# Performance work log

Hardware: AMD Instinct MI355X
Metric: run time of the kernel (lower is better)

## Reference

```python
import jax, jax.numpy as jnp
import numpy as np

BITS, NF, NX = 8, 4096, 1024
G = NX // 8  # groups of 8 weights packed per uint8


def setup_inputs() -> dict:
    key = jax.random.key(0)
    k1, k2, k3, k4 = jax.random.split(key, 4)
    x = jax.random.normal(k1, (2, 2048, NX), dtype=jnp.float32)
    # packed sign bytes per (bit-plane, out-feature, group-of-8 inputs)
    binary = jax.random.randint(k2, (BITS, NF, G), 0, 256, dtype=jnp.int32)
    # per-bit-plane, per-output-row scale (always positive in the sup/l2 schemes)
    scale = jax.random.uniform(k3, (BITS, NF, 1), dtype=jnp.float32)
    bias = jax.random.normal(k4, (NF,), dtype=jnp.float32)
    return {"x": x, "binary": binary, "scale": scale, "bias": bias}


def _decode_signs(binary):
    # binary_exp in the torch code is [2^7..2^0], so element j of each group of 8
    # is stored in bit (7 - j). map4 maps a set bit -> +1, clear bit -> -1.
    shifts = jnp.arange(7, -1, -1, dtype=binary.dtype)
    bits = (binary[..., None] >> shifts) & 1  # (BITS, NF, G, 8)
    sign = jnp.where(bits == 1, 1.0, -1.0).astype(jnp.float32)
    return sign.reshape(binary.shape[0], binary.shape[1], -1)  # (BITS, NF, NX)


def reference(x, binary, scale, bias):
    # Math of the original forward:
    #   table[t, g, hi, lo] = x[t, 8g:8g+4] . map4[:, hi] + x[t, 8g+4:8g+8] . map4[:, lo]
    #   out[t, f] = sum_i scale[i, f] * sum_g table[t, g, binary[i,f,g]>>4, binary[i,f,g]&15]
    # which is exactly sum_i scale[i,f] * (x[t] . sign_i[f]).  We fold the
    # bit-plane sum into an effective weight and run one dense GEMM.
    size_out = x.shape[:-1] + (scale.shape[1],)
    xf = x.reshape(-1, x.shape[-1])            # (T, NX)
    sign = _decode_signs(binary)               # (BITS, NF, NX), values in {-1,+1}
    W = jnp.einsum('kfn,kfo->fn', sign, scale)  # effective weight (NF, NX)
    out = xf @ W.T + bias                      # (T, NF)
    return out.reshape(size_out)
```

## Files before the change

### kernel.cpp

```cpp
#include <hip/hip_runtime.h>
#include <hip/hip_bf16.h>
#include <stdint.h>


#define BITS 8
#define NF   4096
#define NXX  1024
#define GRP  (NXX / 8)

#define BM 256
#define BN 256
#define BK 64
#define NTHR 512

typedef __attribute__((ext_vector_type(4))) float f32x4;
typedef __attribute__((ext_vector_type(8))) short bf16x8;

__global__ __launch_bounds__(256) void k_prep(const float* __restrict__ x,
                                              const int* __restrict__ binary,
                                              const float* __restrict__ scale,
                                              __hip_bfloat16* __restrict__ xb,
                                              __hip_bfloat16* __restrict__ Wb) {
    const int b = blockIdx.x;
    const int tid = threadIdx.x;
    if (b < 2048) {
        int i = b * 256 + tid;
        const float4* xp = (const float4*)x;
        float4 a = xp[2 * i], c = xp[2 * i + 1];
        union { __hip_bfloat16 h[8]; int4 v; } u;
        u.h[0] = __float2bfloat16(a.x);
        u.h[1] = __float2bfloat16(a.y);
        u.h[2] = __float2bfloat16(a.z);
        u.h[3] = __float2bfloat16(a.w);
        u.h[4] = __float2bfloat16(c.x);
        u.h[5] = __float2bfloat16(c.y);
        u.h[6] = __float2bfloat16(c.z);
        u.h[7] = __float2bfloat16(c.w);
        ((int4*)xb)[i] = u.v;
    } else {
        int idx = (b - 2048) * 256 + tid;
        int f = idx >> 7;
        int g = idx & (GRP - 1);
        float sc[BITS];
        int   bv[BITS];
#pragma unroll
        for (int k = 0; k < BITS; ++k) {
            sc[k] = scale[k * NF + f];
            bv[k] = binary[(size_t)(k * NF + f) * GRP + g];
        }
        union { __hip_bfloat16 h[8]; int4 v; } u;
#pragma unroll
        for (int j = 0; j < 8; ++j) {
            float s = 0.f;
#pragma unroll
            for (int k = 0; k < BITS; ++k)
                s += ((bv[k] >> (7 - j)) & 1) ? sc[k] : -sc[k];
            u.h[j] = __float2bfloat16(s);
        }
        ((int4*)Wb)[idx] = u.v;
    }
}

__global__ __launch_bounds__(NTHR, 2) void k_gemm(const __hip_bfloat16* __restrict__ A,
                                                  const __hip_bfloat16* __restrict__ B,
                                                  const float* __restrict__ bias,
                                                  float* __restrict__ C,
                                                  int M, int N, int K) {
    __shared__ __align__(16) char lds[131072];

    const int tid  = threadIdx.x;
    const int lane = tid & 63;
    const int wid  = tid >> 6;
    const int wm = wid >> 2;
    const int wn = wid & 3;
    const int lr = lane & 15;
    const int lk = lane >> 4;

    const int nwg = gridDim.x;
    const int cpx = nwg >> 3;
    const int bid = blockIdx.x;
    const int swz = (bid & 7) * cpx + (bid >> 3);
    const int m0 = (swz >> 4) * BM;
    const int n0 = (swz & 15) * BN;

    const int NT = K / BK;

    auto stageA = [&](int buf, int kt) {
        const __hip_bfloat16* src = A + (size_t)m0 * K + kt;
        char* dst = lds + buf * 65536;
#pragma unroll
        for (int j = 0; j < 4; ++j) {
            int c = j * 512 + tid;
            int r = c >> 3;
            int q = (c & 7) ^ (r & 7);
            __builtin_amdgcn_global_load_lds(
                (const __attribute__((address_space(1))) void*)(src + (size_t)r * K + q * 8),
                (__attribute__((address_space(3))) void*)(dst + j * 8192 + tid * 16), 16, 0, 0);
        }
    };
    auto stageB = [&](int buf, int kt) {
        const __hip_bfloat16* src = B + (size_t)n0 * K + kt;
        char* dst = lds + buf * 65536 + 32768;
#pragma unroll
        for (int j = 0; j < 4; ++j) {
            int c = j * 512 + tid;
            int r = c >> 3;
            int q = (c & 7) ^ (r & 7);
            __builtin_amdgcn_global_load_lds(
                (const __attribute__((address_space(1))) void*)(src + (size_t)r * K + q * 8),
                (__attribute__((address_space(3))) void*)(dst + j * 8192 + tid * 16), 16, 0, 0);
        }
    };
    auto ldA = [&](int buf, int msub, int i, int kk) -> bf16x8 {
        int R = wm * 128 + msub * 64 + i * 16 + lr;
        int CB = (kk * 64 + lk * 16) ^ ((R & 7) << 4);
        return *(const bf16x8*)(lds + buf * 65536 + R * 128 + CB);
    };
    auto ldB = [&](int buf, int nsub, int j, int kk) -> bf16x8 {
        int R = wn * 64 + nsub * 32 + j * 16 + lr;
        int CB = (kk * 64 + lk * 16) ^ ((R & 7) << 4);
        return *(const bf16x8*)(lds + buf * 65536 + 32768 + R * 128 + CB);
    };

    f32x4 acc[8][4] = {};
    bf16x8 aF[4][2], bF0[2][2], bF1[2][2];

    stageA(0, 0);
    stageB(0, 0);

    for (int t = 0; t < NT; ++t) {
        const int cb = t & 1;
        const bool st = (t + 1 < NT);
        asm volatile("s_waitcnt vmcnt(0)" ::: "memory");
        __builtin_amdgcn_sched_barrier(0);
        __builtin_amdgcn_s_barrier();

#pragma unroll
        for (int i = 0; i < 4; ++i)
#pragma unroll
            for (int kk = 0; kk < 2; ++kk) aF[i][kk] = ldA(cb, 0, i, kk);
#pragma unroll
        for (int j = 0; j < 2; ++j)
#pragma unroll
            for (int kk = 0; kk < 2; ++kk) bF0[j][kk] = ldB(cb, 0, j, kk);
        if (st) stageA(cb ^ 1, (t + 1) * BK);
        __builtin_amdgcn_s_barrier();
        asm volatile("s_waitcnt lgkmcnt(0)" ::: "memory");
        __builtin_amdgcn_sched_barrier(0);
        __builtin_amdgcn_s_setprio(1);
#pragma unroll
        for (int i = 0; i < 4; ++i)
#pragma unroll
            for (int j = 0; j < 2; ++j)
#pragma unroll
                for (int kk = 0; kk < 2; ++kk)
                    acc[i][j] = __builtin_amdgcn_mfma_f32_16x16x32_bf16(aF[i][kk], bF0[j][kk], acc[i][j], 0, 0, 0);
        __builtin_amdgcn_s_setprio(0);
        __builtin_amdgcn_sched_barrier(0);
        __builtin_amdgcn_s_barrier();

#pragma unroll
        for (int j = 0; j < 2; ++j)
#pragma unroll
            for (int kk = 0; kk < 2; ++kk) bF1[j][kk] = ldB(cb, 1, j, kk);
        if (st) stageB(cb ^ 1, (t + 1) * BK);
        __builtin_amdgcn_s_barrier();
        asm volatile("s_waitcnt lgkmcnt(0)" ::: "memory");
        __builtin_amdgcn_sched_barrier(0);
        __builtin_amdgcn_s_setprio(1);
#pragma unroll
        for (int i = 0; i < 4; ++i)
#pragma unroll
            for (int j = 0; j < 2; ++j)
#pragma unroll
                for (int kk = 0; kk < 2; ++kk)
                    acc[i][2 + j] = __builtin_amdgcn_mfma_f32_16x16x32_bf16(aF[i][kk], bF1[j][kk], acc[i][2 + j], 0, 0, 0);
        __builtin_amdgcn_s_setprio(0);
        __builtin_amdgcn_sched_barrier(0);
        __builtin_amdgcn_s_barrier();

#pragma unroll
        for (int i = 0; i < 4; ++i)
#pragma unroll
            for (int kk = 0; kk < 2; ++kk) aF[i][kk] = ldA(cb, 1, i, kk);
        __builtin_amdgcn_s_barrier();
        asm volatile("s_waitcnt lgkmcnt(0)" ::: "memory");
        __builtin_amdgcn_sched_barrier(0);
        __builtin_amdgcn_s_setprio(1);
#pragma unroll
        for (int i = 0; i < 4; ++i)
#pragma unroll
            for (int j = 0; j < 2; ++j)
#pragma unroll
                for (int kk = 0; kk < 2; ++kk)
                    acc[4 + i][j] = __builtin_amdgcn_mfma_f32_16x16x32_bf16(aF[i][kk], bF0[j][kk], acc[4 + i][j], 0, 0, 0);
        __builtin_amdgcn_s_setprio(0);
        __builtin_amdgcn_sched_barrier(0);
        __builtin_amdgcn_s_barrier();

        __builtin_amdgcn_s_setprio(1);
#pragma unroll
        for (int i = 0; i < 4; ++i)
#pragma unroll
            for (int j = 0; j < 2; ++j)
#pragma unroll
                for (int kk = 0; kk < 2; ++kk)
                    acc[4 + i][2 + j] = __builtin_amdgcn_mfma_f32_16x16x32_bf16(aF[i][kk], bF1[j][kk], acc[4 + i][2 + j], 0, 0, 0);
        __builtin_amdgcn_s_setprio(0);
        __builtin_amdgcn_sched_barrier(0);
        __builtin_amdgcn_s_barrier();
    }

#pragma unroll
    for (int j = 0; j < 4; ++j) {
        int col = n0 + wn * 64 + j * 16 + lr;
        float bv = bias[col];
#pragma unroll
        for (int i = 0; i < 8; ++i) {
            int row = m0 + wm * 128 + i * 16 + lk * 4;
#pragma unroll
            for (int r = 0; r < 4; ++r)
                C[(size_t)(row + r) * N + col] = acc[i][j][r] + bv;
        }
    }
}

extern "C" void kernel_launch(void* const* d_in, const int* in_sizes, int n_in,
                              void* d_out, int out_size, void* d_ws, size_t ws_size,
                              hipStream_t stream) {
    const float* x      = (const float*)d_in[0];
    const int*   binary = (const int*)d_in[1];
    const float* scale  = (const float*)d_in[2];
    const float* bias   = (const float*)d_in[3];
    float* out = (float*)d_out;

    const int M = in_sizes[0] / NXX;

    __hip_bfloat16* xb = (__hip_bfloat16*)d_ws;
    __hip_bfloat16* Wb = xb + (size_t)M * NXX;

    k_prep<<<2048 + (NF * GRP) / 256, 256, 0, stream>>>(x, binary, scale, xb, Wb);
    k_gemm<<<(M / BM) * (NF / BN), NTHR, 0, stream>>>(xb, Wb, bias, out, M, NF, NXX);
}
```

Measured before the change: 134.5 us.

## Split tile staging into quarter units and keep loads in flight across iterations

Replaces the per-iteration stageA/stageB with four finer staging units (two A halves, two B halves), each issued as soon as its LDS region has been consumed. The loop is unrolled by two, and the full vmcnt(0) drain is replaced by vmcnt(6), so prefetches for the next tile stay in flight across the barrier. The intent is to hide global-to-LDS latency behind MFMA work instead of stalling at the top of every k-step. The cost is more complex buffer reuse reasoning, where a wrong wait count or ordering would create a data race.

```diff
diff --git a/kernel.cpp b/kernel.cpp
--- a/kernel.cpp
+++ b/kernel.cpp
@@ -84,31 +84,24 @@
     const int n0 = (swz & 15) * BN;
 
     const int NT = K / BK;
-
-    auto stageA = [&](int buf, int kt) {
-        const __hip_bfloat16* src = A + (size_t)m0 * K + kt;
-        char* dst = lds + buf * 65536;
-#pragma unroll
-        for (int j = 0; j < 4; ++j) {
-            int c = j * 512 + tid;
-            int r = c >> 3;
-            int q = (c & 7) ^ (r & 7);
+    const int NI = NT / 2;
+
+    auto stage_unit = [&](int buf, int kt, int kind) {
+        const bool isA = (kind < 2);
+        const __hip_bfloat16* src = (isA ? A + (size_t)m0 * K : B + (size_t)n0 * K) + kt;
+        char* base = lds + buf * 65536 + (isA ? 0 : 32768);
+        int lrr = tid >> 3;
+        int q   = tid & 7;
+        int R0;
+        if (isA) R0 = ((kind == 1) ? 64 : 0) + lrr;
+        else     R0 = ((kind == 3) ? 32 : 0) + (lrr & 31) + ((lrr & 32) << 1);
+#pragma unroll
+        for (int call = 0; call < 2; ++call) {
+            int R  = R0 + call * 128;
+            int qs = q ^ (R & 7);
             __builtin_amdgcn_global_load_lds(
-                (const __attribute__((address_space(1))) void*)(src + (size_t)r * K + q * 8),
-                (__attribute__((address_space(3))) void*)(dst + j * 8192 + tid * 16), 16, 0, 0);
-        }
-    };
-    auto stageB = [&](int buf, int kt) {
-        const __hip_bfloat16* src = B + (size_t)n0 * K + kt;
-        char* dst = lds + buf * 65536 + 32768;
-#pragma unroll
-        for (int j = 0; j < 4; ++j) {
-            int c = j * 512 + tid;
-            int r = c >> 3;
-            int q = (c & 7) ^ (r & 7);
-            __builtin_amdgcn_global_load_lds(
-                (const __attribute__((address_space(1))) void*)(src + (size_t)r * K + q * 8),
-                (__attribute__((address_space(3))) void*)(dst + j * 8192 + tid * 16), 16, 0, 0);
+                (const __attribute__((address_space(1))) void*)(src + (size_t)R * K + qs * 8),
+                (__attribute__((address_space(3))) void*)(base + R * 128 + q * 16), 16, 0, 0);
         }
     };
     auto ldA = [&](int buf, int msub, int i, int kk) -> bf16x8 {
@@ -125,91 +118,80 @@
     f32x4 acc[8][4] = {};
     bf16x8 aF[4][2], bF0[2][2], bF1[2][2];
 
-    stageA(0, 0);
-    stageB(0, 0);
-
-    for (int t = 0; t < NT; ++t) {
-        const int cb = t & 1;
-        const bool st = (t + 1 < NT);
-        asm volatile("s_waitcnt vmcnt(0)" ::: "memory");
-        __builtin_amdgcn_sched_barrier(0);
-        __builtin_amdgcn_s_barrier();
-
-#pragma unroll
-        for (int i = 0; i < 4; ++i)
-#pragma unroll
-            for (int kk = 0; kk < 2; ++kk) aF[i][kk] = ldA(cb, 0, i, kk);
-#pragma unroll
-        for (int j = 0; j < 2; ++j)
-#pragma unroll
-            for (int kk = 0; kk < 2; ++kk) bF0[j][kk] = ldB(cb, 0, j, kk);
-        if (st) stageA(cb ^ 1, (t + 1) * BK);
-        __builtin_amdgcn_s_barrier();
-        asm volatile("s_waitcnt lgkmcnt(0)" ::: "memory");
-        __builtin_amdgcn_sched_barrier(0);
-        __builtin_amdgcn_s_setprio(1);
-#pragma unroll
-        for (int i = 0; i < 4; ++i)
-#pragma unroll
-            for (int j = 0; j < 2; ++j)
-#pragma unroll
-                for (int kk = 0; kk < 2; ++kk)
-                    acc[i][j] = __builtin_amdgcn_mfma_f32_16x16x32_bf16(aF[i][kk], bF0[j][kk], acc[i][j], 0, 0, 0);
-        __builtin_amdgcn_s_setprio(0);
-        __builtin_amdgcn_sched_barrier(0);
-        __builtin_amdgcn_s_barrier();
-
-#pragma unroll
-        for (int j = 0; j < 2; ++j)
-#pragma unroll
-            for (int kk = 0; kk < 2; ++kk) bF1[j][kk] = ldB(cb, 1, j, kk);
-        if (st) stageB(cb ^ 1, (t + 1) * BK);
-        __builtin_amdgcn_s_barrier();
-        asm volatile("s_waitcnt lgkmcnt(0)" ::: "memory");
-        __builtin_amdgcn_sched_barrier(0);
-        __builtin_amdgcn_s_setprio(1);
-#pragma unroll
-        for (int i = 0; i < 4; ++i)
-#pragma unroll
-            for (int j = 0; j < 2; ++j)
-#pragma unroll
-                for (int kk = 0; kk < 2; ++kk)
-                    acc[i][2 + j] = __builtin_amdgcn_mfma_f32_16x16x32_bf16(aF[i][kk], bF1[j][kk], acc[i][2 + j], 0, 0, 0);
-        __builtin_amdgcn_s_setprio(0);
-        __builtin_amdgcn_sched_barrier(0);
-        __builtin_amdgcn_s_barrier();
-
-#pragma unroll
-        for (int i = 0; i < 4; ++i)
-#pragma unroll
-            for (int kk = 0; kk < 2; ++kk) aF[i][kk] = ldA(cb, 1, i, kk);
-        __builtin_amdgcn_s_barrier();
-        asm volatile("s_waitcnt lgkmcnt(0)" ::: "memory");
-        __builtin_amdgcn_sched_barrier(0);
-        __builtin_amdgcn_s_setprio(1);
-#pragma unroll
-        for (int i = 0; i < 4; ++i)
-#pragma unroll
-            for (int j = 0; j < 2; ++j)
-#pragma unroll
-                for (int kk = 0; kk < 2; ++kk)
-                    acc[4 + i][j] = __builtin_amdgcn_mfma_f32_16x16x32_bf16(aF[i][kk], bF0[j][kk], acc[4 + i][j], 0, 0, 0);
-        __builtin_amdgcn_s_setprio(0);
-        __builtin_amdgcn_sched_barrier(0);
-        __builtin_amdgcn_s_barrier();
-
-        __builtin_amdgcn_s_setprio(1);
-#pragma unroll
-        for (int i = 0; i < 4; ++i)
-#pragma unroll
-            for (int j = 0; j < 2; ++j)
-#pragma unroll
-                for (int kk = 0; kk < 2; ++kk)
-                    acc[4 + i][2 + j] = __builtin_amdgcn_mfma_f32_16x16x32_bf16(aF[i][kk], bF1[j][kk], acc[4 + i][2 + j], 0, 0, 0);
-        __builtin_amdgcn_s_setprio(0);
-        __builtin_amdgcn_sched_barrier(0);
-        __builtin_amdgcn_s_barrier();
+#define BAR()   __builtin_amdgcn_s_barrier()
+#define LGKM0() do { asm volatile("s_waitcnt lgkmcnt(0)" ::: "memory"); \
+                     __builtin_amdgcn_sched_barrier(0); } while (0)
+#define VM6()   do { __builtin_amdgcn_sched_barrier(0); \
+                     asm volatile("s_waitcnt vmcnt(6)" ::: "memory"); } while (0)
+#define PRIO1() __builtin_amdgcn_s_setprio(1)
+#define PRIO0() do { __builtin_amdgcn_s_setprio(0); \
+                     __builtin_amdgcn_sched_barrier(0); } while (0)
+#define MFMA_Q(ms, ns, BF)                                                         \
+    do {                                                                           \
+        _Pragma("unroll") for (int i = 0; i < 4; ++i)                              \
+        _Pragma("unroll") for (int j = 0; j < 2; ++j)                              \
+        _Pragma("unroll") for (int kk = 0; kk < 2; ++kk)                           \
+            acc[(ms)*4 + i][(ns)*2 + j] = __builtin_amdgcn_mfma_f32_16x16x32_bf16( \
+                aF[i][kk], BF[j][kk], acc[(ms)*4 + i][(ns)*2 + j], 0, 0, 0);       \
+    } while (0)
+
+    stage_unit(0, 0, 0); stage_unit(0, 0, 2); stage_unit(0, 0, 3); stage_unit(0, 0, 1);
+    stage_unit(1, BK, 2); stage_unit(1, BK, 3); stage_unit(1, BK, 1);
+    asm volatile("s_waitcnt vmcnt(6)" ::: "memory");
+    BAR();
+
+    for (int it = 0; it < NI; ++it) {
+        const int to = 2 * it + 1;
+        const int tn = 2 * it + 2;
+        const bool st = (it + 1 < NI);
+
+#pragma unroll
+        for (int i = 0; i < 4; ++i) { aF[i][0] = ldA(0, 0, i, 0); aF[i][1] = ldA(0, 0, i, 1); }
+#pragma unroll
+        for (int j = 0; j < 2; ++j) { bF0[j][0] = ldB(0, 0, j, 0); bF0[j][1] = ldB(0, 0, j, 1); }
+        stage_unit(1, to * BK, 0);
+        BAR(); LGKM0(); PRIO1(); MFMA_Q(0, 0, bF0); PRIO0(); BAR();
+
+#pragma unroll
+        for (int j = 0; j < 2; ++j) { bF1[j][0] = ldB(0, 1, j, 0); bF1[j][1] = ldB(0, 1, j, 1); }
+        if (st) stage_unit(0, tn * BK, 2);
+        BAR(); LGKM0(); PRIO1(); MFMA_Q(0, 1, bF1); PRIO0(); BAR();
+
+#pragma unroll
+        for (int i = 0; i < 4; ++i) { aF[i][0] = ldA(0, 1, i, 0); aF[i][1] = ldA(0, 1, i, 1); }
+        if (st) stage_unit(0, tn * BK, 3);
+        BAR(); LGKM0(); PRIO1(); MFMA_Q(1, 0, bF0); PRIO0(); BAR();
+
+        if (st) stage_unit(0, tn * BK, 1);
+        BAR(); PRIO1(); MFMA_Q(1, 1, bF1); PRIO0(); VM6(); BAR();
+
+#pragma unroll
+        for (int i = 0; i < 4; ++i) { aF[i][0] = ldA(1, 0, i, 0); aF[i][1] = ldA(1, 0, i, 1); }
+#pragma unroll
+        for (int j = 0; j < 2; ++j) { bF0[j][0] = ldB(1, 0, j, 0); bF0[j][1] = ldB(1, 0, j, 1); }
+        if (st) stage_unit(0, tn * BK, 0);
+        BAR(); LGKM0(); PRIO1(); MFMA_Q(0, 0, bF0); PRIO0(); BAR();
+
+#pragma unroll
+        for (int j = 0; j < 2; ++j) { bF1[j][0] = ldB(1, 1, j, 0); bF1[j][1] = ldB(1, 1, j, 1); }
+        if (st) stage_unit(1, (tn + 1) * BK, 2);
+        BAR(); LGKM0(); PRIO1(); MFMA_Q(0, 1, bF1); PRIO0(); BAR();
+
+#pragma unroll
+        for (int i = 0; i < 4; ++i) { aF[i][0] = ldA(1, 1, i, 0); aF[i][1] = ldA(1, 1, i, 1); }
+        if (st) stage_unit(1, (tn + 1) * BK, 3);
+        BAR(); LGKM0(); PRIO1(); MFMA_Q(1, 0, bF0); PRIO0(); BAR();
+
+        if (st) stage_unit(1, (tn + 1) * BK, 1);
+        BAR(); PRIO1(); MFMA_Q(1, 1, bF1); PRIO0(); VM6(); BAR();
     }
+
+#undef BAR
+#undef LGKM0
+#undef VM6
+#undef PRIO1
+#undef PRIO0
+#undef MFMA_Q
 
 #pragma unroll
     for (int j = 0; j < 4; ++j) {
```

Result: no change. 133.1 us (-1.1%).
